# Kernel optimization log

Measured on AMD Instinct MI355X. Metric: run time of the kernel, lower is better.

Reference implementation:

```python
import jax, jax.numpy as jnp
import numpy as np

N, D = 768, 64
EPS = 1e-5

def _ln(x, g, b):
    u = x.mean(-1, keepdims=True)
    s = ((x - u) ** 2).mean(-1, keepdims=True)
    return g * (x - u) / jnp.sqrt(s + EPS) + b

def setup_inputs() -> dict:
    key = jax.random.key(0)
    ks = jax.random.split(key, 16)
    inp = {
        'corr_index': jax.random.normal(ks[0], (N, N, 2), dtype=jnp.float32),
        'nei_index': jax.random.randint(ks[1], (N, N), 0, 2, dtype=jnp.int32),
        'nei_num': jax.random.randint(ks[2], (N,), 0, N, dtype=jnp.int32),
        'hidden_state': jax.random.normal(ks[3], (N, D), dtype=jnp.float32),
        'cn': jax.random.normal(ks[4], (N, D), dtype=jnp.float32),
        # relativeLayer: MLP(2 -> D)
        'W_r': jax.random.normal(ks[5], (2, D)) * 0.01, 'b_r': jnp.zeros((D,)),
        'g_r': jnp.ones((D,)), 'be_r': jax.random.normal(ks[6], (D,)) * 0.02,
        # ngate: MLP_gate(3D -> D)
        'W_g': jax.random.normal(ks[7], (3 * D, D)) * 0.01, 'b_g': jnp.zeros((D,)),
        'g_g': jnp.ones((D,)), 'be_g': jax.random.normal(ks[8], (D,)) * 0.02,
        # WAr: MLP(3D -> 1)
        'W_a': jax.random.normal(ks[9], (3 * D, 1)) * 0.01, 'b_a': jnp.zeros((1,)),
        'g_a': jnp.ones((1,)), 'be_a': jnp.abs(jax.random.normal(ks[10], (1,))) * 0.02 + 0.01,
        # weight: MLP(D -> D)
        'W_w': jax.random.normal(ks[11], (D, D)) * 0.01, 'b_w': jnp.zeros((D,)),
        'g_w': jnp.ones((D,)), 'be_w': jax.random.normal(ks[12], (D,)) * 0.02,
    }
    return inp

def reference(corr_index, nei_index, nei_num, hidden_state, cn,
              W_r, b_r, g_r, be_r, W_g, b_g, g_g, be_g,
              W_a, b_a, g_a, be_a, W_w, b_w, g_w, be_w):
    n, d = hidden_state.shape
    mask = nei_index > 0  # [N,N]; (i,j): j is neighbor of i
    # relativeLayer on all pairs (values at masked positions match the torch gather)
    r = jax.nn.relu(_ln(corr_index @ W_r + b_r, g_r, be_r))  # [N,N,D]
    hi = jnp.broadcast_to(hidden_state[:, None, :], (n, n, d))  # hi_t: h[i]
    hj = jnp.broadcast_to(hidden_state[None, :, :], (n, n, d))  # nei_inputs: h[j]
    tmp = jnp.concatenate([r, hi, hj], axis=-1)  # [N,N,3D]
    nGate = jax.nn.sigmoid(_ln(tmp @ W_g + b_g, g_g, be_g))  # [N,N,D]
    tt = jax.nn.relu(_ln(tmp @ W_a + b_a, g_a, be_a))[..., 0]  # [N,N]
    Pos = jnp.where(mask, tt, 0.0)
    Pos = jnp.where(Pos == 0.0, -10000.0, Pos)  # Pos[Pos==0] = -10000
    Pos = jax.nn.softmax(Pos, axis=1)  # masked row-softmax over neighbors j
    # H[i,j] = h[j] * nGate[i,j] * Pos[i,j] at masked pairs, else 0
    H = jnp.where(mask[..., None], hj * nGate * Pos[..., None], 0.0)
    H_sum = jax.nn.relu(_ln(jnp.sum(H, axis=1) @ W_w + b_w, g_w, be_w))  # [N,D]
    C = H_sum + cn
    H_out = hidden_state + jnp.tanh(C)
    return (H_out, C)
```

## Files before the change

kernel.cpp:

```cpp
#include <hip/hip_runtime.h>


#define NN 768
#define DD 64
#define EPSF 1e-5f

typedef __attribute__((ext_vector_type(8))) short short8;
typedef __attribute__((ext_vector_type(4))) float float4v;

__device__ __forceinline__ unsigned short f2bf(float f) {
  unsigned int u = __float_as_uint(f);
  u += 0x7fffu + ((u >> 16) & 1u);
  return (unsigned short)(u >> 16);
}

__global__ __launch_bounds__(64) void prep_kernel(
    const float* __restrict__ hidden, const float* __restrict__ Wg,
    const float* __restrict__ bg, const float* __restrict__ Wr,
    const float* __restrict__ br, float* __restrict__ A_pre,
    float* __restrict__ B_pre, float* __restrict__ w0h,
    float* __restrict__ w1h, float* __restrict__ bh,
    float* __restrict__ evec) {
  const int t = threadIdx.x;
  const int i = blockIdx.x;
  if (i < NN) {
    float hv = hidden[i * DD + t];
    float a = bg[t];
    float b = 0.f;
#pragma unroll 8
    for (int k = 0; k < DD; ++k) {
      float hk = __shfl(hv, k);
      a = fmaf(hk, Wg[(DD + k) * DD + t], a);
      b = fmaf(hk, Wg[(2 * DD + k) * DD + t], b);
    }
    A_pre[i * DD + t] = a;
    B_pre[i * DD + t] = b;
  } else {
    float w0 = Wr[t], w1 = Wr[DD + t], bb = br[t];
    float m0 = w0, m1 = w1, mb = bb;
    for (int m = 1; m < 64; m <<= 1) {
      m0 += __shfl_xor(m0, m);
      m1 += __shfl_xor(m1, m);
      mb += __shfl_xor(mb, m);
    }
    m0 *= (1.f / DD);
    m1 *= (1.f / DD);
    mb *= (1.f / DD);
    float a0 = w0 - m0, a1 = w1 - m1, ab = bb - mb;
    w0h[t] = a0;
    w1h[t] = a1;
    bh[t] = ab;
    float e00 = a0 * a0, e11 = a1 * a1, ebb = ab * ab;
    float e01 = a0 * a1, e0b = a0 * ab, e1b = a1 * ab;
    for (int m = 1; m < 64; m <<= 1) {
      e00 += __shfl_xor(e00, m);
      e11 += __shfl_xor(e11, m);
      ebb += __shfl_xor(ebb, m);
      e01 += __shfl_xor(e01, m);
      e0b += __shfl_xor(e0b, m);
      e1b += __shfl_xor(e1b, m);
    }
    if (t == 0) {
      evec[0] = e00 * (1.f / DD);
      evec[1] = e11 * (1.f / DD);
      evec[2] = ebb * (1.f / DD);
      evec[3] = e01 * (1.f / DD);
      evec[4] = e0b * (1.f / DD);
      evec[5] = e1b * (1.f / DD);
    }
  }
}

__global__ __launch_bounds__(256) void gatraj_main(
    const float* __restrict__ corr, const int* __restrict__ nei,
    const float* __restrict__ hidden, const float* __restrict__ cn,
    const float* __restrict__ gr, const float* __restrict__ ber,
    const float* __restrict__ Wg, const float* __restrict__ gg,
    const float* __restrict__ beg, const float* __restrict__ bea,
    const float* __restrict__ Ww, const float* __restrict__ bw,
    const float* __restrict__ gw, const float* __restrict__ bew,
    const float* __restrict__ A_pre, const float* __restrict__ B_pre,
    const float* __restrict__ w0h, const float* __restrict__ w1h,
    const float* __restrict__ bh, const float* __restrict__ evec,
    float* __restrict__ out) {
  __shared__ __align__(16) unsigned short Rt[64 * 72];
  __shared__ short Lst[NN];
  __shared__ short jpc[64];
  __shared__ float4v cpk[64];
  __shared__ float red[4 * 64];
  __shared__ int cntLds;

  const int i = blockIdx.x;
  const int tid = threadIdx.x;
  const int wid = tid >> 6;
  const int lane = tid & 63;
  const int quad = lane >> 4;
  const int nl = lane & 15;

  if (tid == 0) cntLds = 0;
  __syncthreads();
#pragma unroll
  for (int rep = 0; rep < 3; ++rep) {
    int jj = tid + rep * 256;
    if (nei[i * NN + jj] > 0) {
      int idx = atomicAdd(&cntLds, 1);
      Lst[idx] = (short)jj;
    }
  }

  const float pgr = gr[lane];
  const float gw0 = pgr * w0h[lane];
  const float gw1 = pgr * w1h[lane];
  const float gbh = pgr * bh[lane];
  const float pber = ber[lane];
  const float e00 = evec[0], e11 = evec[1], ebb = evec[2];
  const float e01 = evec[3], e0b = evec[4], e1b = evec[5];

  float gg4[4], beg4[4], pre4[4];
#pragma unroll
  for (int nt = 0; nt < 4; ++nt) {
    int d = nt * 16 + nl;
    gg4[nt] = gg[d];
    beg4[nt] = beg[d];
    pre4[nt] = A_pre[i * DD + d];
  }

  short8 Bf[2][4];
#pragma unroll
  for (int ks = 0; ks < 2; ++ks)
#pragma unroll
    for (int nt = 0; nt < 4; ++nt) {
      short8 f;
#pragma unroll
      for (int e = 0; e < 8; ++e) {
        int k = ks * 32 + quad * 8 + e;
        f[e] = (short)f2bf(Wg[k * DD + nt * 16 + nl]);
      }
      Bf[ks][nt] = f;
    }

  __syncthreads();
  const int cnt = cntLds;

  float accT[4] = {0.f, 0.f, 0.f, 0.f};

  for (int base = 0; base < cnt; base += 64) {
    __syncthreads();
    if (wid == 0) {
      int pg = base + lane;
      int jp = (pg < cnt) ? (int)Lst[pg] : (int)Lst[0];
      jpc[lane] = (short)jp;
      float c0 = corr[(i * NN + jp) * 2 + 0];
      float c1 = corr[(i * NN + jp) * 2 + 1];
      float var = c0 * c0 * e00 + c1 * c1 * e11 + ebb +
                  2.f * (c0 * c1 * e01 + c0 * e0b + c1 * e1b);
      float4v v;
      v[0] = c0;
      v[1] = c1;
      v[2] = rsqrtf(var + EPSF);
      v[3] = 0.f;
      cpk[lane] = v;
    }
    __syncthreads();

    float4v myc = cpk[wid * 16 + nl];
#pragma unroll
    for (int q = 0; q < 16; ++q) {
      int p = wid * 16 + q;
      float c0 = __shfl(myc[0], q);
      float c1 = __shfl(myc[1], q);
      float iv = __shfl(myc[2], q);
      float s3 = fmaf(c0, gw0, fmaf(c1, gw1, gbh));
      float r = fmaxf(0.f, fmaf(iv, s3, pber));
      Rt[p * 72 + lane] = f2bf(r);
    }

    short8 a0, a1;
    __builtin_memcpy(&a0, &Rt[(wid * 16 + nl) * 72 + quad * 8], 16);
    __builtin_memcpy(&a1, &Rt[(wid * 16 + nl) * 72 + 32 + quad * 8], 16);
    float4v acc[4];
#pragma unroll
    for (int nt = 0; nt < 4; ++nt) {
      float4v z = {0.f, 0.f, 0.f, 0.f};
      z = __builtin_amdgcn_mfma_f32_16x16x32_bf16(a0, Bf[0][nt], z, 0, 0, 0);
      z = __builtin_amdgcn_mfma_f32_16x16x32_bf16(a1, Bf[1][nt], z, 0, 0, 0);
      acc[nt] = z;
    }

    int jpr[4];
    float pv[4];
#pragma unroll
    for (int rr = 0; rr < 4; ++rr) {
      int pl = wid * 16 + quad * 4 + rr;
      jpr[rr] = (int)jpc[pl];
      pv[rr] = (base + pl < cnt) ? 1.f : 0.f;
    }
    float y[4][4];
#pragma unroll
    for (int nt = 0; nt < 4; ++nt)
#pragma unroll
      for (int rr = 0; rr < 4; ++rr)
        y[nt][rr] = acc[nt][rr] + pre4[nt] + B_pre[jpr[rr] * DD + nt * 16 + nl];
#pragma unroll
    for (int rr = 0; rr < 4; ++rr) {
      float s = y[0][rr] + y[1][rr] + y[2][rr] + y[3][rr];
      float qq = y[0][rr] * y[0][rr] + y[1][rr] * y[1][rr] +
                 y[2][rr] * y[2][rr] + y[3][rr] * y[3][rr];
#pragma unroll
      for (int m = 1; m < 16; m <<= 1) {
        s += __shfl_xor(s, m);
        qq += __shfl_xor(qq, m);
      }
      float u = s * (1.f / DD);
      float var = qq * (1.f / DD) - u * u;
      float inv = rsqrtf(var + EPSF);
      int jj = jpr[rr];
#pragma unroll
      for (int nt = 0; nt < 4; ++nt) {
        float g = fmaf(gg4[nt], (y[nt][rr] - u) * inv, beg4[nt]);
        float gate = __frcp_rn(1.f + __expf(-g));
        float hval = hidden[jj * DD + nt * 16 + nl];
        accT[nt] = fmaf(gate * pv[rr], hval, accT[nt]);
      }
    }
  }

#pragma unroll
  for (int nt = 0; nt < 4; ++nt) {
    accT[nt] += __shfl_xor(accT[nt], 16);
    accT[nt] += __shfl_xor(accT[nt], 32);
  }
  if (lane < 16) {
#pragma unroll
    for (int nt = 0; nt < 4; ++nt) red[wid * 64 + nt * 16 + lane] = accT[nt];
  }
  __syncthreads();

  if (tid < 64) {
    int d = tid;
    float hs = red[d] + red[64 + d] + red[128 + d] + red[192 + d];
    float tta = fmaxf(bea[0], 0.f);
    float wgt = (tta > 0.f && cnt > 0) ? (1.f / (float)cnt) : (1.f / (float)NN);
    hs *= wgt;
    float dotv = bw[d];
#pragma unroll 8
    for (int k = 0; k < DD; ++k) {
      float hk = __shfl(hs, k);
      dotv = fmaf(hk, Ww[k * DD + d], dotv);
    }
    float s = dotv, qq = dotv * dotv;
#pragma unroll
    for (int m = 1; m < 64; m <<= 1) {
      s += __shfl_xor(s, m);
      qq += __shfl_xor(qq, m);
    }
    float u = s * (1.f / DD);
    float var = qq * (1.f / DD) - u * u;
    float inv = rsqrtf(var + EPSF);
    float val = fmaxf(0.f, fmaf(gw[d], (dotv - u) * inv, bew[d]));
    float Cv = val + cn[i * DD + d];
    float Ho = hidden[i * DD + d] + tanhf(Cv);
    out[i * DD + d] = Ho;
    out[NN * DD + i * DD + d] = Cv;
  }
}

extern "C" void kernel_launch(void* const* d_in, const int* in_sizes, int n_in,
                              void* d_out, int out_size, void* d_ws,
                              size_t ws_size, hipStream_t stream) {
  const float* corr = (const float*)d_in[0];
  const int* nei = (const int*)d_in[1];
  const float* hidden = (const float*)d_in[3];
  const float* cn = (const float*)d_in[4];
  const float* Wr = (const float*)d_in[5];
  const float* br = (const float*)d_in[6];
  const float* gr = (const float*)d_in[7];
  const float* ber = (const float*)d_in[8];
  const float* Wg = (const float*)d_in[9];
  const float* bg = (const float*)d_in[10];
  const float* gg = (const float*)d_in[11];
  const float* beg = (const float*)d_in[12];
  const float* bea = (const float*)d_in[16];
  const float* Ww = (const float*)d_in[17];
  const float* bw = (const float*)d_in[18];
  const float* gw = (const float*)d_in[19];
  const float* bew = (const float*)d_in[20];
  float* out = (float*)d_out;

  float* ws = (float*)d_ws;
  float* A_pre = ws;
  float* B_pre = ws + NN * DD;
  float* w0h = ws + 2 * NN * DD;
  float* w1h = w0h + 64;
  float* bh = w0h + 128;
  float* evec = w0h + 192;

  prep_kernel<<<NN + 1, 64, 0, stream>>>(hidden, Wg, bg, Wr, br, A_pre, B_pre,
                                         w0h, w1h, bh, evec);
  gatraj_main<<<NN, 256, 0, stream>>>(corr, nei, hidden, cn, gr, ber, Wg, gg,
                                      beg, bea, Ww, bw, gw, bew, A_pre, B_pre,
                                      w0h, w1h, bh, evec, out);
}
```

Baseline: 135.2 us.

## Split per-row neighbor loop into chunked pair blocks with separate reduction kernel

```diff
diff --git a/kernel.cpp b/kernel.cpp
--- a/kernel.cpp
+++ b/kernel.cpp
@@ -3,6 +3,7 @@
 
 #define NN 768
 #define DD 64
+#define NCH 12
 #define EPSF 1e-5f
 
 typedef __attribute__((ext_vector_type(8))) short short8;
@@ -14,107 +15,141 @@
   return (unsigned short)(u >> 16);
 }
 
-__global__ __launch_bounds__(64) void prep_kernel(
+__global__ __launch_bounds__(256) void prep_kernel(
     const float* __restrict__ hidden, const float* __restrict__ Wg,
     const float* __restrict__ bg, const float* __restrict__ Wr,
-    const float* __restrict__ br, float* __restrict__ A_pre,
-    float* __restrict__ B_pre, float* __restrict__ w0h,
-    float* __restrict__ w1h, float* __restrict__ bh,
-    float* __restrict__ evec) {
-  const int t = threadIdx.x;
-  const int i = blockIdx.x;
-  if (i < NN) {
-    float hv = hidden[i * DD + t];
-    float a = bg[t];
-    float b = 0.f;
+    const float* __restrict__ br, const int* __restrict__ nei,
+    float* __restrict__ A_pre, float* __restrict__ B_pre,
+    float* __restrict__ w0h, float* __restrict__ w1h, float* __restrict__ bh,
+    float* __restrict__ evec, unsigned short* __restrict__ WgT,
+    unsigned short* __restrict__ Lst, int* __restrict__ cnt_g) {
+  const int bid = blockIdx.x;
+  const int tid = threadIdx.x;
+
+  if (bid < NN) {
+    __shared__ int cLds;
+    if (tid == 0) cLds = 0;
+    __syncthreads();
+#pragma unroll
+    for (int rep = 0; rep < 3; ++rep) {
+      int jj = tid + rep * 256;
+      if (nei[bid * NN + jj] > 0) {
+        int idx = atomicAdd(&cLds, 1);
+        Lst[bid * NN + idx] = (unsigned short)jj;
+      }
+    }
+    __syncthreads();
+    if (tid == 0) cnt_g[bid] = cLds;
+    return;
+  }
+
+  if (bid == NN) {
+    for (int idx = tid; idx < DD * DD; idx += 256) {
+      int n = idx >> 6, k = idx & 63;
+      WgT[idx] = f2bf(Wg[k * DD + n]);
+    }
+    if (tid < 64) {
+      int t = tid;
+      float w0 = Wr[t], w1 = Wr[DD + t], bb = br[t];
+      float m0 = w0, m1 = w1, mb = bb;
+      for (int m = 1; m < 64; m <<= 1) {
+        m0 += __shfl_xor(m0, m);
+        m1 += __shfl_xor(m1, m);
+        mb += __shfl_xor(mb, m);
+      }
+      m0 *= (1.f / DD);
+      m1 *= (1.f / DD);
+      mb *= (1.f / DD);
+      float a0 = w0 - m0, a1 = w1 - m1, ab = bb - mb;
+      w0h[t] = a0;
+      w1h[t] = a1;
+      bh[t] = ab;
+      float e00 = a0 * a0, e11 = a1 * a1, ebb = ab * ab;
+      float e01 = a0 * a1, e0b = a0 * ab, e1b = a1 * ab;
+      for (int m = 1; m < 64; m <<= 1) {
+        e00 += __shfl_xor(e00, m);
+        e11 += __shfl_xor(e11, m);
+        ebb += __shfl_xor(ebb, m);
+        e01 += __shfl_xor(e01, m);
+        e0b += __shfl_xor(e0b, m);
+        e1b += __shfl_xor(e1b, m);
+      }
+      if (t == 0) {
+        evec[0] = e00 * (1.f / DD);
+        evec[1] = e11 * (1.f / DD);
+        evec[2] = ebb * (1.f / DD);
+        evec[3] = e01 * (1.f / DD);
+        evec[4] = e0b * (1.f / DD);
+        evec[5] = e1b * (1.f / DD);
+      }
+    }
+    return;
+  }
+
+  const int w = tid >> 6;
+  const int lane = tid & 63;
+  const int i = (bid - NN - 1) * 4 + w;
+  float hv = hidden[i * DD + lane];
+  float a = bg[lane];
+  float b = 0.f;
 #pragma unroll 8
-    for (int k = 0; k < DD; ++k) {
-      float hk = __shfl(hv, k);
-      a = fmaf(hk, Wg[(DD + k) * DD + t], a);
-      b = fmaf(hk, Wg[(2 * DD + k) * DD + t], b);
-    }
-    A_pre[i * DD + t] = a;
-    B_pre[i * DD + t] = b;
-  } else {
-    float w0 = Wr[t], w1 = Wr[DD + t], bb = br[t];
-    float m0 = w0, m1 = w1, mb = bb;
-    for (int m = 1; m < 64; m <<= 1) {
-      m0 += __shfl_xor(m0, m);
-      m1 += __shfl_xor(m1, m);
-      mb += __shfl_xor(mb, m);
-    }
-    m0 *= (1.f / DD);
-    m1 *= (1.f / DD);
-    mb *= (1.f / DD);
-    float a0 = w0 - m0, a1 = w1 - m1, ab = bb - mb;
-    w0h[t] = a0;
-    w1h[t] = a1;
-    bh[t] = ab;
-    float e00 = a0 * a0, e11 = a1 * a1, ebb = ab * ab;
-    float e01 = a0 * a1, e0b = a0 * ab, e1b = a1 * ab;
-    for (int m = 1; m < 64; m <<= 1) {
-      e00 += __shfl_xor(e00, m);
-      e11 += __shfl_xor(e11, m);
-      ebb += __shfl_xor(ebb, m);
-      e01 += __shfl_xor(e01, m);
-      e0b += __shfl_xor(e0b, m);
-      e1b += __shfl_xor(e1b, m);
-    }
-    if (t == 0) {
-      evec[0] = e00 * (1.f / DD);
-      evec[1] = e11 * (1.f / DD);
-      evec[2] = ebb * (1.f / DD);
-      evec[3] = e01 * (1.f / DD);
-      evec[4] = e0b * (1.f / DD);
-      evec[5] = e1b * (1.f / DD);
-    }
-  }
-}
-
-__global__ __launch_bounds__(256) void gatraj_main(
-    const float* __restrict__ corr, const int* __restrict__ nei,
-    const float* __restrict__ hidden, const float* __restrict__ cn,
+  for (int k = 0; k < DD; ++k) {
+    float hk = __shfl(hv, k);
+    a = fmaf(hk, Wg[(DD + k) * DD + lane], a);
+    b = fmaf(hk, Wg[(2 * DD + k) * DD + lane], b);
+  }
+  A_pre[i * DD + lane] = a;
+  B_pre[i * DD + lane] = b;
+}
+
+__global__ __launch_bounds__(64) void pair_kernel(
+    const float* __restrict__ corr, const float* __restrict__ hidden,
     const float* __restrict__ gr, const float* __restrict__ ber,
-    const float* __restrict__ Wg, const float* __restrict__ gg,
-    const float* __restrict__ beg, const float* __restrict__ bea,
-    const float* __restrict__ Ww, const float* __restrict__ bw,
-    const float* __restrict__ gw, const float* __restrict__ bew,
+    const float* __restrict__ gg, const float* __restrict__ beg,
     const float* __restrict__ A_pre, const float* __restrict__ B_pre,
     const float* __restrict__ w0h, const float* __restrict__ w1h,
     const float* __restrict__ bh, const float* __restrict__ evec,
-    float* __restrict__ out) {
-  __shared__ __align__(16) unsigned short Rt[64 * 72];
-  __shared__ short Lst[NN];
-  __shared__ short jpc[64];
-  __shared__ float4v cpk[64];
-  __shared__ float red[4 * 64];
-  __shared__ int cntLds;
-
-  const int i = blockIdx.x;
-  const int tid = threadIdx.x;
-  const int wid = tid >> 6;
-  const int lane = tid & 63;
+    const unsigned short* __restrict__ WgT,
+    const unsigned short* __restrict__ Lst, const int* __restrict__ cnt_g,
+    float* __restrict__ Hpart) {
+  const int bid = blockIdx.x;
+  const int i = bid / NCH;
+  const int c = bid - i * NCH;
+  const int cnt = cnt_g[i];
+  const int base = c * 64;
+  if (base >= cnt) return;
+
+  const int lane = threadIdx.x;
   const int quad = lane >> 4;
   const int nl = lane & 15;
 
-  if (tid == 0) cntLds = 0;
-  __syncthreads();
-#pragma unroll
-  for (int rep = 0; rep < 3; ++rep) {
-    int jj = tid + rep * 256;
-    if (nei[i * NN + jj] > 0) {
-      int idx = atomicAdd(&cntLds, 1);
-      Lst[idx] = (short)jj;
-    }
-  }
+  __shared__ __align__(16) unsigned short Rt[64 * 72];
+  __shared__ int jpc[64];
+
+  int pg = base + lane;
+  int jp = (int)Lst[i * NN + (pg < cnt ? pg : base)];
+  jpc[lane] = jp;
+  float c0 = corr[(i * NN + jp) * 2 + 0];
+  float c1 = corr[(i * NN + jp) * 2 + 1];
+  const float e00 = evec[0], e11 = evec[1], ebb = evec[2];
+  const float e01 = evec[3], e0b = evec[4], e1b = evec[5];
+  float var = c0 * c0 * e00 + c1 * c1 * e11 + ebb +
+              2.f * (c0 * c1 * e01 + c0 * e0b + c1 * e1b);
+  float iv = rsqrtf(var + EPSF);
 
   const float pgr = gr[lane];
   const float gw0 = pgr * w0h[lane];
   const float gw1 = pgr * w1h[lane];
   const float gbh = pgr * bh[lane];
   const float pber = ber[lane];
-  const float e00 = evec[0], e11 = evec[1], ebb = evec[2];
-  const float e01 = evec[3], e0b = evec[4], e1b = evec[5];
+
+  short8 Bf[2][4];
+#pragma unroll
+  for (int ks = 0; ks < 2; ++ks)
+#pragma unroll
+    for (int nt = 0; nt < 4; ++nt)
+      __builtin_memcpy(&Bf[ks][nt], &WgT[(nt * 16 + nl) * DD + ks * 32 + quad * 8],
+                       16);
 
   float gg4[4], beg4[4], pre4[4];
 #pragma unroll
@@ -125,59 +160,24 @@
     pre4[nt] = A_pre[i * DD + d];
   }
 
-  short8 Bf[2][4];
-#pragma unroll
-  for (int ks = 0; ks < 2; ++ks)
-#pragma unroll
-    for (int nt = 0; nt < 4; ++nt) {
-      short8 f;
-#pragma unroll
-      for (int e = 0; e < 8; ++e) {
-        int k = ks * 32 + quad * 8 + e;
-        f[e] = (short)f2bf(Wg[k * DD + nt * 16 + nl]);
-      }
-      Bf[ks][nt] = f;
-    }
-
+#pragma unroll
+  for (int p = 0; p < 64; ++p) {
+    float sc0 = __shfl(c0, p);
+    float sc1 = __shfl(c1, p);
+    float siv = __shfl(iv, p);
+    float s3 = fmaf(sc0, gw0, fmaf(sc1, gw1, gbh));
+    float r = fmaxf(0.f, fmaf(siv, s3, pber));
+    Rt[p * 72 + lane] = f2bf(r);
+  }
   __syncthreads();
-  const int cnt = cntLds;
 
   float accT[4] = {0.f, 0.f, 0.f, 0.f};
 
-  for (int base = 0; base < cnt; base += 64) {
-    __syncthreads();
-    if (wid == 0) {
-      int pg = base + lane;
-      int jp = (pg < cnt) ? (int)Lst[pg] : (int)Lst[0];
-      jpc[lane] = (short)jp;
-      float c0 = corr[(i * NN + jp) * 2 + 0];
-      float c1 = corr[(i * NN + jp) * 2 + 1];
-      float var = c0 * c0 * e00 + c1 * c1 * e11 + ebb +
-                  2.f * (c0 * c1 * e01 + c0 * e0b + c1 * e1b);
-      float4v v;
-      v[0] = c0;
-      v[1] = c1;
-      v[2] = rsqrtf(var + EPSF);
-      v[3] = 0.f;
-      cpk[lane] = v;
-    }
-    __syncthreads();
-
-    float4v myc = cpk[wid * 16 + nl];
-#pragma unroll
-    for (int q = 0; q < 16; ++q) {
-      int p = wid * 16 + q;
-      float c0 = __shfl(myc[0], q);
-      float c1 = __shfl(myc[1], q);
-      float iv = __shfl(myc[2], q);
-      float s3 = fmaf(c0, gw0, fmaf(c1, gw1, gbh));
-      float r = fmaxf(0.f, fmaf(iv, s3, pber));
-      Rt[p * 72 + lane] = f2bf(r);
-    }
-
+#pragma unroll
+  for (int t = 0; t < 4; ++t) {
     short8 a0, a1;
-    __builtin_memcpy(&a0, &Rt[(wid * 16 + nl) * 72 + quad * 8], 16);
-    __builtin_memcpy(&a1, &Rt[(wid * 16 + nl) * 72 + 32 + quad * 8], 16);
+    __builtin_memcpy(&a0, &Rt[(t * 16 + nl) * 72 + quad * 8], 16);
+    __builtin_memcpy(&a1, &Rt[(t * 16 + nl) * 72 + 32 + quad * 8], 16);
     float4v acc[4];
 #pragma unroll
     for (int nt = 0; nt < 4; ++nt) {
@@ -191,8 +191,8 @@
     float pv[4];
 #pragma unroll
     for (int rr = 0; rr < 4; ++rr) {
-      int pl = wid * 16 + quad * 4 + rr;
-      jpr[rr] = (int)jpc[pl];
+      int pl = t * 16 + quad * 4 + rr;
+      jpr[rr] = jpc[pl];
       pv[rr] = (base + pl < cnt) ? 1.f : 0.f;
     }
     float y[4][4];
@@ -212,8 +212,8 @@
         qq += __shfl_xor(qq, m);
       }
       float u = s * (1.f / DD);
-      float var = qq * (1.f / DD) - u * u;
-      float inv = rsqrtf(var + EPSF);
+      float vv = qq * (1.f / DD) - u * u;
+      float inv = rsqrtf(vv + EPSF);
       int jj = jpr[rr];
 #pragma unroll
       for (int nt = 0; nt < 4; ++nt) {
@@ -232,37 +232,47 @@
   }
   if (lane < 16) {
 #pragma unroll
-    for (int nt = 0; nt < 4; ++nt) red[wid * 64 + nt * 16 + lane] = accT[nt];
-  }
-  __syncthreads();
-
-  if (tid < 64) {
-    int d = tid;
-    float hs = red[d] + red[64 + d] + red[128 + d] + red[192 + d];
-    float tta = fmaxf(bea[0], 0.f);
-    float wgt = (tta > 0.f && cnt > 0) ? (1.f / (float)cnt) : (1.f / (float)NN);
-    hs *= wgt;
-    float dotv = bw[d];
+    for (int nt = 0; nt < 4; ++nt)
+      Hpart[bid * DD + nt * 16 + nl] = accT[nt];
+  }
+}
+
+__global__ __launch_bounds__(64) void final_kernel(
+    const float* __restrict__ hidden, const float* __restrict__ cn,
+    const float* __restrict__ bea, const float* __restrict__ Ww,
+    const float* __restrict__ bw, const float* __restrict__ gw,
+    const float* __restrict__ bew, const int* __restrict__ cnt_g,
+    const float* __restrict__ Hpart, float* __restrict__ out) {
+  const int i = blockIdx.x;
+  const int d = threadIdx.x;
+  const int cnt = cnt_g[i];
+  const int nch = (cnt + 63) >> 6;
+  float hs = 0.f;
+  for (int c = 0; c < nch; ++c) hs += Hpart[(i * NCH + c) * DD + d];
+  float tta = fmaxf(bea[0], 0.f);
+  float wgt = (tta > 0.f && cnt > 0) ? (1.f / (float)cnt) : (1.f / (float)NN);
+  hs *= wgt;
+
+  float dotv = bw[d];
 #pragma unroll 8
-    for (int k = 0; k < DD; ++k) {
-      float hk = __shfl(hs, k);
-      dotv = fmaf(hk, Ww[k * DD + d], dotv);
-    }
-    float s = dotv, qq = dotv * dotv;
-#pragma unroll
-    for (int m = 1; m < 64; m <<= 1) {
-      s += __shfl_xor(s, m);
-      qq += __shfl_xor(qq, m);
-    }
-    float u = s * (1.f / DD);
-    float var = qq * (1.f / DD) - u * u;
-    float inv = rsqrtf(var + EPSF);
-    float val = fmaxf(0.f, fmaf(gw[d], (dotv - u) * inv, bew[d]));
-    float Cv = val + cn[i * DD + d];
-    float Ho = hidden[i * DD + d] + tanhf(Cv);
-    out[i * DD + d] = Ho;
-    out[NN * DD + i * DD + d] = Cv;
-  }
+  for (int k = 0; k < DD; ++k) {
+    float hk = __shfl(hs, k);
+    dotv = fmaf(hk, Ww[k * DD + d], dotv);
+  }
+  float s = dotv, qq = dotv * dotv;
+#pragma unroll
+  for (int m = 1; m < 64; m <<= 1) {
+    s += __shfl_xor(s, m);
+    qq += __shfl_xor(qq, m);
+  }
+  float u = s * (1.f / DD);
+  float var = qq * (1.f / DD) - u * u;
+  float inv = rsqrtf(var + EPSF);
+  float val = fmaxf(0.f, fmaf(gw[d], (dotv - u) * inv, bew[d]));
+  float Cv = val + cn[i * DD + d];
+  float Ho = hidden[i * DD + d] + tanhf(Cv);
+  out[i * DD + d] = Ho;
+  out[NN * DD + i * DD + d] = Cv;
 }
 
 extern "C" void kernel_launch(void* const* d_in, const int* in_sizes, int n_in,
@@ -289,15 +299,22 @@
 
   float* ws = (float*)d_ws;
   float* A_pre = ws;
-  float* B_pre = ws + NN * DD;
-  float* w0h = ws + 2 * NN * DD;
-  float* w1h = w0h + 64;
-  float* bh = w0h + 128;
-  float* evec = w0h + 192;
-
-  prep_kernel<<<NN + 1, 64, 0, stream>>>(hidden, Wg, bg, Wr, br, A_pre, B_pre,
-                                         w0h, w1h, bh, evec);
-  gatraj_main<<<NN, 256, 0, stream>>>(corr, nei, hidden, cn, gr, ber, Wg, gg,
-                                      beg, bea, Ww, bw, gw, bew, A_pre, B_pre,
-                                      w0h, w1h, bh, evec, out);
-}
+  float* B_pre = ws + 49152;
+  float* w0h = ws + 98304;
+  float* w1h = ws + 98368;
+  float* bh = ws + 98432;
+  float* evec = ws + 98496;
+  unsigned short* WgT = (unsigned short*)(ws + 98512);
+  int* cnt_g = (int*)(ws + 100560);
+  unsigned short* Lst = (unsigned short*)(ws + 101328);
+  float* Hpart = ws + 396240;
+
+  prep_kernel<<<NN + 1 + NN / 4, 256, 0, stream>>>(
+      hidden, Wg, bg, Wr, br, nei, A_pre, B_pre, w0h, w1h, bh, evec, WgT, Lst,
+      cnt_g);
+  pair_kernel<<<NN * NCH, 64, 0, stream>>>(corr, hidden, gr, ber, gg, beg,
+                                           A_pre, B_pre, w0h, w1h, bh, evec,
+                                           WgT, Lst, cnt_g, Hpart);
+  final_kernel<<<NN, 64, 0, stream>>>(hidden, cn, bea, Ww, bw, gw, bew, cnt_g,
+                                      Hpart, out);
+}
```

New measurement: 141.2 us. +4.4%, slower.
